# Optimization experiments

Measured on AMD Instinct MI355X. Metric: run time of the kernel, lower is better.

The kernel has to match this reference:

```python
import jax, jax.numpy as jnp
import numpy as np

# metaLinearLayer: per-sample weight W_b = left^T @ diag(meta_b) @ right.
# torch builds diag(meta)@eye@left then transposes and matmuls right, i.e.
# meta_weight[b] = (diag(meta_b) @ left).T @ right, shape (input_dim, out_dim).
# We apply it via associativity: (x @ left^T) * meta, then @ right -- same math,
# skipping the dense per-sample weight.

B, S, D_IN, D_OUT, P = 8, 4096, 2048, 2048, 256

def setup_inputs() -> dict:
    key = jax.random.key(0)
    ks = jax.random.split(key, 6)
    scale_l = (6.0 / D_IN) ** 0.5   # kaiming_uniform-ish magnitude
    scale_r = (6.0 / P) ** 0.5
    return {
        "input": jax.random.normal(ks[0], (B, S, D_IN), dtype=jnp.float32),
        "meta_input": jax.random.normal(ks[1], (B, P), dtype=jnp.float32),
        "left": jax.random.uniform(ks[2], (P, D_IN), dtype=jnp.float32, minval=-scale_l, maxval=scale_l),
        "right": jax.random.uniform(ks[3], (P, D_OUT), dtype=jnp.float32, minval=-scale_r, maxval=scale_r),
        "bias_w": jax.random.uniform(ks[4], (P, D_OUT), dtype=jnp.float32, minval=-scale_r, maxval=scale_r),
        "bias_b": jax.random.uniform(ks[5], (D_OUT,), dtype=jnp.float32, minval=-scale_r, maxval=scale_r),
    }

def reference(input, meta_input, left, right, bias_w, bias_b):
    # project input to rank-P space: [B,S,P]
    h = jnp.einsum('bsj,pj->bsp', input, left)
    # per-sample diagonal scaling by meta_input
    h = h * meta_input[:, None, :]
    # project to out_dim: [B,S,out_dim]
    out = jnp.einsum('bsp,pk->bsk', h, right)
    # meta bias = project2bias(meta_input), broadcast over seq
    meta_bias = meta_input @ bias_w + bias_b  # [B, out_dim]
    return out + meta_bias[:, None, :]
```

## Files before the change

### kernel.cpp

```cpp
#include <hip/hip_runtime.h>
#include <hip/hip_bf16.h>

#define B_    8
#define S_    4096
#define DIN   2048
#define DOUT  2048
#define P_    256
#define M_    (B_ * S_)

typedef __attribute__((ext_vector_type(4))) float f32x4;
typedef __attribute__((ext_vector_type(8))) short bf16x8;
typedef __attribute__((ext_vector_type(4))) short bf16x4;

static __device__ __forceinline__ short f2bs(float x) {
    __hip_bfloat16 h = __float2bfloat16(x);
    return *reinterpret_cast<short*>(&h);
}

__global__ __launch_bounds__(256)
void cvt_bf16_kernel(const float* __restrict__ src, short* __restrict__ dst, int n8) {
    int i = blockIdx.x * 256 + threadIdx.x;
    if (i >= n8) return;
    const float4* s = reinterpret_cast<const float4*>(src) + (size_t)i * 2;
    float4 a = s[0], b = s[1];
    bf16x8 o;
    o[0] = f2bs(a.x); o[1] = f2bs(a.y); o[2] = f2bs(a.z); o[3] = f2bs(a.w);
    o[4] = f2bs(b.x); o[5] = f2bs(b.y); o[6] = f2bs(b.z); o[7] = f2bs(b.w);
    *(reinterpret_cast<bf16x8*>(dst) + i) = o;
}

__global__ __launch_bounds__(256)
void transposeR_kernel(const float* __restrict__ R, short* __restrict__ Rt) {
    __shared__ float T[64][65];
    const int n0 = blockIdx.x * 64;
    const int k0 = blockIdx.y * 64;
    const int tid = threadIdx.x;
    #pragma unroll
    for (int e = 0; e < 16; ++e) {
        int idx = tid + e * 256;
        int r = idx >> 6, c = idx & 63;
        T[r][c] = R[(size_t)(k0 + r) * DOUT + n0 + c];
    }
    __syncthreads();
    #pragma unroll
    for (int e = 0; e < 4; ++e) {
        int g = tid + e * 256;
        int n = g >> 4, k4 = (g & 15) << 2;
        bf16x4 v;
        v[0] = f2bs(T[k4 + 0][n]); v[1] = f2bs(T[k4 + 1][n]);
        v[2] = f2bs(T[k4 + 2][n]); v[3] = f2bs(T[k4 + 3][n]);
        *reinterpret_cast<bf16x4*>(&Rt[(size_t)(n0 + n) * P_ + k0 + k4]) = v;
    }
}

__global__ __launch_bounds__(256)
void meta_bias_kernel(const float* __restrict__ meta,
                      const float* __restrict__ bias_w,
                      const float* __restrict__ bias_b,
                      float* __restrict__ mb) {
    int idx = blockIdx.x * 256 + threadIdx.x;
    int b = idx / DOUT;
    int k = idx - b * DOUT;
    const float* mrow = meta + b * P_;
    float acc = bias_b[k];
    #pragma unroll 8
    for (int p = 0; p < P_; ++p)
        acc = fmaf(mrow[p], bias_w[p * DOUT + k], acc);
    mb[idx] = acc;
}

template<int KTOT, int LDC, bool A_F32, bool META_EPI>
__global__ __launch_bounds__(512, 2)
void gemm_bt(const void* __restrict__ Ap,
             const short* __restrict__ Bp,
             const float* __restrict__ vvec,
             void* __restrict__ Cp) {
    constexpr int BM = 128, BN = 256, BK = 64;
    __shared__ short As[BM * BK];
    __shared__ short Bs[BN * BK];

    const int tid  = threadIdx.x;
    const int lane = tid & 63;
    const int w    = tid >> 6;
    const int wr   = w >> 2;
    const int wc   = w & 3;
    const int lm   = lane & 15;
    const int rg   = lane >> 4;
    const int r0   = blockIdx.x * BM;
    const int c0   = blockIdx.y * BN;
    const int bidx = r0 / S_;

    f32x4 acc[4][4] = {};

    const float* Af = (const float*)Ap;
    const short* Ab = (const short*)Ap;

    for (int k0 = 0; k0 < KTOT; k0 += BK) {
        #pragma unroll
        for (int e = 0; e < 2; ++e) {
            int c   = tid + e * 512;
            int row = c >> 3;
            int k8  = (c & 7) << 3;
            int off = ((row * BK + k8) * 2) ^ ((row & 7) << 4);
            bf16x8 o;
            if (A_F32) {
                const float* src = Af + (size_t)(r0 + row) * KTOT + k0 + k8;
                float4 v0 = *reinterpret_cast<const float4*>(src);
                float4 v1 = *reinterpret_cast<const float4*>(src + 4);
                o[0] = f2bs(v0.x); o[1] = f2bs(v0.y); o[2] = f2bs(v0.z); o[3] = f2bs(v0.w);
                o[4] = f2bs(v1.x); o[5] = f2bs(v1.y); o[6] = f2bs(v1.z); o[7] = f2bs(v1.w);
            } else {
                o = *reinterpret_cast<const bf16x8*>(Ab + (size_t)(r0 + row) * KTOT + k0 + k8);
            }
            *reinterpret_cast<bf16x8*>(reinterpret_cast<char*>(As) + off) = o;
        }
        #pragma unroll
        for (int e = 0; e < 4; ++e) {
            int c   = tid + e * 512;
            int row = c >> 3;
            int k8  = (c & 7) << 3;
            int off = ((row * BK + k8) * 2) ^ ((row & 7) << 4);
            bf16x8 o = *reinterpret_cast<const bf16x8*>(Bp + (size_t)(c0 + row) * KTOT + k0 + k8);
            *reinterpret_cast<bf16x8*>(reinterpret_cast<char*>(Bs) + off) = o;
        }
        __syncthreads();

        bf16x8 af[4][2], bfr[4][2];
        #pragma unroll
        for (int i = 0; i < 4; ++i)
            #pragma unroll
            for (int kk = 0; kk < 2; ++kk) {
                int m   = wr * 64 + i * 16 + lm;
                int off = ((m * BK + kk * 32 + rg * 8) * 2) ^ ((m & 7) << 4);
                af[i][kk] = *reinterpret_cast<const bf16x8*>(reinterpret_cast<const char*>(As) + off);
            }
        #pragma unroll
        for (int j = 0; j < 4; ++j)
            #pragma unroll
            for (int kk = 0; kk < 2; ++kk) {
                int n   = wc * 64 + j * 16 + lm;
                int off = ((n * BK + kk * 32 + rg * 8) * 2) ^ ((n & 7) << 4);
                bfr[j][kk] = *reinterpret_cast<const bf16x8*>(reinterpret_cast<const char*>(Bs) + off);
            }
        #pragma unroll
        for (int kk = 0; kk < 2; ++kk)
            #pragma unroll
            for (int i = 0; i < 4; ++i)
                #pragma unroll
                for (int j = 0; j < 4; ++j)
                    acc[i][j] = __builtin_amdgcn_mfma_f32_16x16x32_bf16(
                        af[i][kk], bfr[j][kk], acc[i][j], 0, 0, 0);
        __syncthreads();
    }

    if (META_EPI) {
        const float* mrow = vvec + bidx * P_;
        short* Hc = (short*)Cp;
        #pragma unroll
        for (int i = 0; i < 4; ++i) {
            int rbase = r0 + wr * 64 + i * 16 + rg * 4;
            #pragma unroll
            for (int j = 0; j < 4; ++j) {
                int col = c0 + wc * 64 + j * 16 + lm;
                float mv = mrow[col];
                #pragma unroll
                for (int q = 0; q < 4; ++q)
                    Hc[(size_t)(rbase + q) * LDC + col] = f2bs(acc[i][j][q] * mv);
            }
        }
    } else {
        const float* mbr = vvec + bidx * DOUT;
        float* Oc = (float*)Cp;
        #pragma unroll
        for (int i = 0; i < 4; ++i) {
            int rbase = r0 + wr * 64 + i * 16 + rg * 4;
            #pragma unroll
            for (int j = 0; j < 4; ++j) {
                int col = c0 + wc * 64 + j * 16 + lm;
                float bv = mbr[col];
                #pragma unroll
                for (int q = 0; q < 4; ++q)
                    Oc[(size_t)(rbase + q) * LDC + col] = acc[i][j][q] + bv;
            }
        }
    }
}

extern "C" void kernel_launch(void* const* d_in, const int* in_sizes, int n_in,
                              void* d_out, int out_size, void* d_ws, size_t ws_size,
                              hipStream_t stream) {
    const float* input  = (const float*)d_in[0];
    const float* meta   = (const float*)d_in[1];
    const float* left   = (const float*)d_in[2];
    const float* right  = (const float*)d_in[3];
    const float* bias_w = (const float*)d_in[4];
    const float* bias_b = (const float*)d_in[5];
    float* out = (float*)d_out;

    char* ws = (char*)d_ws;
    short* H  = (short*)ws;
    float* mb = (float*)(ws + 16777216);
    short* Lb = (short*)(ws + 16777216 + 65536);
    short* Rt = (short*)(ws + 16777216 + 65536 + 1048576);

    cvt_bf16_kernel<<<256, 256, 0, stream>>>(left, Lb, (P_ * DIN) / 8);
    transposeR_kernel<<<dim3(DOUT / 64, P_ / 64), 256, 0, stream>>>(right, Rt);
    meta_bias_kernel<<<(B_ * DOUT) / 256, 256, 0, stream>>>(meta, bias_w, bias_b, mb);

    gemm_bt<DIN, P_, true, true>
        <<<dim3(M_ / 128, 1), 512, 0, stream>>>(input, Lb, meta, H);

    gemm_bt<P_, DOUT, false, false>
        <<<dim3(M_ / 128, DOUT / 256), 512, 0, stream>>>(H, Rt, mb, out);
}
```

Before: 593.3 us.

## Pre-swizzle weight and H tiles and stream them with direct global-to-LDS loads

Weights and the intermediate H are written in a pre-tiled, pre-swizzled image layout, so the GEMM can copy 32KB/8KB tiles straight into LDS with global_load_lds instead of going through registers. The GEMM block shrinks to 64x256 with 256 threads at occupancy 3, and the meta-bias kernel is vectorised to float4. This removes register staging and address math for the B and H operands. In exchange the stage-1 GEMM now reads the whole left matrix for every 64 rows instead of every 128, and the stage-2 grid has twice as many blocks.

```diff
diff --git a/kernel.cpp b/kernel.cpp
--- a/kernel.cpp
+++ b/kernel.cpp
@@ -1,5 +1,6 @@
 #include <hip/hip_runtime.h>
 #include <hip/hip_bf16.h>
+#include <stdint.h>
 
 #define B_    8
 #define S_    4096
@@ -10,46 +11,62 @@
 
 typedef __attribute__((ext_vector_type(4))) float f32x4;
 typedef __attribute__((ext_vector_type(8))) short bf16x8;
-typedef __attribute__((ext_vector_type(4))) short bf16x4;
 
 static __device__ __forceinline__ short f2bs(float x) {
     __hip_bfloat16 h = __float2bfloat16(x);
     return *reinterpret_cast<short*>(&h);
 }
 
+static __device__ __forceinline__ void gld_lds16(const void* g, void* l) {
+    __builtin_amdgcn_global_load_lds(
+        (const __attribute__((address_space(1))) unsigned int*)(uintptr_t)g,
+        (__attribute__((address_space(3))) unsigned int*)(uintptr_t)l,
+        16, 0, 0);
+}
+
+#define SWZ(row, byteoff) ((byteoff) ^ (((row) & 7) << 4))
+
 __global__ __launch_bounds__(256)
-void cvt_bf16_kernel(const float* __restrict__ src, short* __restrict__ dst, int n8) {
-    int i = blockIdx.x * 256 + threadIdx.x;
-    if (i >= n8) return;
-    const float4* s = reinterpret_cast<const float4*>(src) + (size_t)i * 2;
-    float4 a = s[0], b = s[1];
+void prep_left(const float* __restrict__ L, char* __restrict__ Lsw) {
+    int g = blockIdx.x * 256 + threadIdx.x;
+    int row = g >> 8;
+    int c8  = g & 255;
+    int k = c8 * 8, kt = k >> 6, kk = k & 63;
+    const float* src = L + (size_t)row * DIN + k;
+    float4 v0 = *reinterpret_cast<const float4*>(src);
+    float4 v1 = *reinterpret_cast<const float4*>(src + 4);
     bf16x8 o;
-    o[0] = f2bs(a.x); o[1] = f2bs(a.y); o[2] = f2bs(a.z); o[3] = f2bs(a.w);
-    o[4] = f2bs(b.x); o[5] = f2bs(b.y); o[6] = f2bs(b.z); o[7] = f2bs(b.w);
-    *(reinterpret_cast<bf16x8*>(dst) + i) = o;
+    o[0]=f2bs(v0.x); o[1]=f2bs(v0.y); o[2]=f2bs(v0.z); o[3]=f2bs(v0.w);
+    o[4]=f2bs(v1.x); o[5]=f2bs(v1.y); o[6]=f2bs(v1.z); o[7]=f2bs(v1.w);
+    int off = kt * 32768 + SWZ(row, row * 128 + kk * 2);
+    *reinterpret_cast<bf16x8*>(Lsw + off) = o;
 }
 
 __global__ __launch_bounds__(256)
-void transposeR_kernel(const float* __restrict__ R, short* __restrict__ Rt) {
+void prep_right(const float* __restrict__ R, char* __restrict__ Rsw) {
     __shared__ float T[64][65];
     const int n0 = blockIdx.x * 64;
-    const int k0 = blockIdx.y * 64;
+    const int p0 = blockIdx.y * 64;
     const int tid = threadIdx.x;
     #pragma unroll
     for (int e = 0; e < 16; ++e) {
         int idx = tid + e * 256;
         int r = idx >> 6, c = idx & 63;
-        T[r][c] = R[(size_t)(k0 + r) * DOUT + n0 + c];
+        T[r][c] = R[(size_t)(p0 + r) * DOUT + n0 + c];
     }
     __syncthreads();
     #pragma unroll
-    for (int e = 0; e < 4; ++e) {
-        int g = tid + e * 256;
-        int n = g >> 4, k4 = (g & 15) << 2;
-        bf16x4 v;
-        v[0] = f2bs(T[k4 + 0][n]); v[1] = f2bs(T[k4 + 1][n]);
-        v[2] = f2bs(T[k4 + 2][n]); v[3] = f2bs(T[k4 + 3][n]);
-        *reinterpret_cast<bf16x4*>(&Rt[(size_t)(n0 + n) * P_ + k0 + k4]) = v;
+    for (int e = 0; e < 2; ++e) {
+        int cc = tid + e * 256;
+        int nl = cc >> 3, p8 = (cc & 7) * 8;
+        bf16x8 o;
+        #pragma unroll
+        for (int u = 0; u < 8; ++u) o[u] = f2bs(T[p8 + u][nl]);
+        int n = n0 + nl;
+        int nb = n >> 8, row = n & 255;
+        int kt = p0 >> 6, kk = p8;
+        int off = (nb * 4 + kt) * 32768 + SWZ(row, row * 128 + kk * 2);
+        *reinterpret_cast<bf16x8*>(Rsw + off) = o;
     }
 }
 
@@ -58,129 +75,138 @@
                       const float* __restrict__ bias_w,
                       const float* __restrict__ bias_b,
                       float* __restrict__ mb) {
-    int idx = blockIdx.x * 256 + threadIdx.x;
-    int b = idx / DOUT;
-    int k = idx - b * DOUT;
+    int g = blockIdx.x * 256 + threadIdx.x;
+    int b  = g >> 9;
+    int k4 = (g & 511) * 4;
     const float* mrow = meta + b * P_;
-    float acc = bias_b[k];
-    #pragma unroll 8
-    for (int p = 0; p < P_; ++p)
-        acc = fmaf(mrow[p], bias_w[p * DOUT + k], acc);
-    mb[idx] = acc;
-}
-
-template<int KTOT, int LDC, bool A_F32, bool META_EPI>
-__global__ __launch_bounds__(512, 2)
-void gemm_bt(const void* __restrict__ Ap,
-             const short* __restrict__ Bp,
-             const float* __restrict__ vvec,
-             void* __restrict__ Cp) {
-    constexpr int BM = 128, BN = 256, BK = 64;
-    __shared__ short As[BM * BK];
-    __shared__ short Bs[BN * BK];
+    float4 acc = *reinterpret_cast<const float4*>(&bias_b[k4]);
+    #pragma unroll 4
+    for (int p = 0; p < P_; ++p) {
+        float mval = mrow[p];
+        float4 wv = *reinterpret_cast<const float4*>(&bias_w[(size_t)p * DOUT + k4]);
+        acc.x = fmaf(mval, wv.x, acc.x);
+        acc.y = fmaf(mval, wv.y, acc.y);
+        acc.z = fmaf(mval, wv.z, acc.z);
+        acc.w = fmaf(mval, wv.w, acc.w);
+    }
+    *reinterpret_cast<float4*>(&mb[(size_t)b * DOUT + k4]) = acc;
+}
+
+template<bool S1>
+__global__ __launch_bounds__(256, 3)
+void gemm_mfma(const void* __restrict__ Ap,
+               const char* __restrict__ Bsw,
+               const float* __restrict__ vvec,
+               void* __restrict__ Cp) {
+    constexpr int KTOT = S1 ? DIN : P_;
+    constexpr int NK   = KTOT / 64;
+    __shared__ short As[64 * 64];
+    __shared__ short Bs[256 * 64];
 
     const int tid  = threadIdx.x;
     const int lane = tid & 63;
     const int w    = tid >> 6;
-    const int wr   = w >> 2;
-    const int wc   = w & 3;
     const int lm   = lane & 15;
     const int rg   = lane >> 4;
-    const int r0   = blockIdx.x * BM;
-    const int c0   = blockIdx.y * BN;
-    const int bidx = r0 / S_;
+    const int mblk = blockIdx.x;
+    const int r0   = mblk * 64;
+    const int c0   = S1 ? 0 : blockIdx.y * 256;
+    const int bidx = mblk >> 6;
 
     f32x4 acc[4][4] = {};
-
-    const float* Af = (const float*)Ap;
-    const short* Ab = (const short*)Ap;
-
-    for (int k0 = 0; k0 < KTOT; k0 += BK) {
-        #pragma unroll
-        for (int e = 0; e < 2; ++e) {
-            int c   = tid + e * 512;
-            int row = c >> 3;
-            int k8  = (c & 7) << 3;
-            int off = ((row * BK + k8) * 2) ^ ((row & 7) << 4);
-            bf16x8 o;
-            if (A_F32) {
-                const float* src = Af + (size_t)(r0 + row) * KTOT + k0 + k8;
+    const float* Xf  = (const float*)Ap;
+    const char* Himg = (const char*)Ap;
+    char* AsB = (char*)As;
+    char* BsB = (char*)Bs;
+
+    for (int kt = 0; kt < NK; ++kt) {
+        const char* bimg = Bsw + (size_t)(S1 ? kt : ((int)blockIdx.y * NK + kt)) * 32768;
+        #pragma unroll
+        for (int c = 0; c < 8; ++c)
+            gld_lds16(bimg + (w * 8 + c) * 1024 + lane * 16, BsB + (w * 8 + c) * 1024);
+        if (S1) {
+            #pragma unroll
+            for (int e = 0; e < 2; ++e) {
+                int row = (tid >> 3) + e * 32;
+                int k8  = (tid & 7) * 8;
+                const float* src = Xf + (size_t)(r0 + row) * DIN + kt * 64 + k8;
                 float4 v0 = *reinterpret_cast<const float4*>(src);
                 float4 v1 = *reinterpret_cast<const float4*>(src + 4);
-                o[0] = f2bs(v0.x); o[1] = f2bs(v0.y); o[2] = f2bs(v0.z); o[3] = f2bs(v0.w);
-                o[4] = f2bs(v1.x); o[5] = f2bs(v1.y); o[6] = f2bs(v1.z); o[7] = f2bs(v1.w);
-            } else {
-                o = *reinterpret_cast<const bf16x8*>(Ab + (size_t)(r0 + row) * KTOT + k0 + k8);
-            }
-            *reinterpret_cast<bf16x8*>(reinterpret_cast<char*>(As) + off) = o;
-        }
-        #pragma unroll
-        for (int e = 0; e < 4; ++e) {
-            int c   = tid + e * 512;
-            int row = c >> 3;
-            int k8  = (c & 7) << 3;
-            int off = ((row * BK + k8) * 2) ^ ((row & 7) << 4);
-            bf16x8 o = *reinterpret_cast<const bf16x8*>(Bp + (size_t)(c0 + row) * KTOT + k0 + k8);
-            *reinterpret_cast<bf16x8*>(reinterpret_cast<char*>(Bs) + off) = o;
+                bf16x8 o;
+                o[0]=f2bs(v0.x); o[1]=f2bs(v0.y); o[2]=f2bs(v0.z); o[3]=f2bs(v0.w);
+                o[4]=f2bs(v1.x); o[5]=f2bs(v1.y); o[6]=f2bs(v1.z); o[7]=f2bs(v1.w);
+                *reinterpret_cast<bf16x8*>(AsB + SWZ(row, row * 128 + k8 * 2)) = o;
+            }
+        } else {
+            const char* aimg = Himg + ((size_t)mblk * NK + kt) * 8192;
+            #pragma unroll
+            for (int c = 0; c < 2; ++c)
+                gld_lds16(aimg + (w * 2 + c) * 1024 + lane * 16, AsB + (w * 2 + c) * 1024);
         }
         __syncthreads();
 
-        bf16x8 af[4][2], bfr[4][2];
-        #pragma unroll
-        for (int i = 0; i < 4; ++i)
-            #pragma unroll
-            for (int kk = 0; kk < 2; ++kk) {
-                int m   = wr * 64 + i * 16 + lm;
-                int off = ((m * BK + kk * 32 + rg * 8) * 2) ^ ((m & 7) << 4);
-                af[i][kk] = *reinterpret_cast<const bf16x8*>(reinterpret_cast<const char*>(As) + off);
-            }
-        #pragma unroll
-        for (int j = 0; j < 4; ++j)
-            #pragma unroll
-            for (int kk = 0; kk < 2; ++kk) {
-                int n   = wc * 64 + j * 16 + lm;
-                int off = ((n * BK + kk * 32 + rg * 8) * 2) ^ ((n & 7) << 4);
-                bfr[j][kk] = *reinterpret_cast<const bf16x8*>(reinterpret_cast<const char*>(Bs) + off);
-            }
-        #pragma unroll
-        for (int kk = 0; kk < 2; ++kk)
+        #pragma unroll
+        for (int kk = 0; kk < 2; ++kk) {
+            bf16x8 af[4], bfr[4];
+            #pragma unroll
+            for (int i = 0; i < 4; ++i) {
+                int m = i * 16 + lm;
+                af[i] = *reinterpret_cast<const bf16x8*>(
+                    AsB + SWZ(m, m * 128 + (kk * 32 + rg * 8) * 2));
+            }
+            #pragma unroll
+            for (int j = 0; j < 4; ++j) {
+                int n = w * 64 + j * 16 + lm;
+                bfr[j] = *reinterpret_cast<const bf16x8*>(
+                    BsB + SWZ(n, n * 128 + (kk * 32 + rg * 8) * 2));
+            }
             #pragma unroll
             for (int i = 0; i < 4; ++i)
                 #pragma unroll
                 for (int j = 0; j < 4; ++j)
                     acc[i][j] = __builtin_amdgcn_mfma_f32_16x16x32_bf16(
-                        af[i][kk], bfr[j][kk], acc[i][j], 0, 0, 0);
+                        af[i], bfr[j], acc[i][j], 0, 0, 0);
+        }
         __syncthreads();
     }
 
-    if (META_EPI) {
+    if (S1) {
         const float* mrow = vvec + bidx * P_;
-        short* Hc = (short*)Cp;
+        char* Hout = (char*)Cp + (size_t)mblk * 32768;
+        float mv[4];
+        #pragma unroll
+        for (int j = 0; j < 4; ++j) mv[j] = mrow[w * 64 + j * 16 + lm];
         #pragma unroll
         for (int i = 0; i < 4; ++i) {
-            int rbase = r0 + wr * 64 + i * 16 + rg * 4;
+            int rb = i * 16 + rg * 4;
             #pragma unroll
             for (int j = 0; j < 4; ++j) {
-                int col = c0 + wc * 64 + j * 16 + lm;
-                float mv = mrow[col];
+                int p = w * 64 + j * 16 + lm;
+                int ktile = p >> 6, kk = p & 63;
                 #pragma unroll
-                for (int q = 0; q < 4; ++q)
-                    Hc[(size_t)(rbase + q) * LDC + col] = f2bs(acc[i][j][q] * mv);
+                for (int q = 0; q < 4; ++q) {
+                    int r = rb + q;
+                    int off = ktile * 8192 + SWZ(r, r * 128 + kk * 2);
+                    *reinterpret_cast<short*>(Hout + off) = f2bs(acc[i][j][q] * mv[j]);
+                }
             }
         }
     } else {
         const float* mbr = vvec + bidx * DOUT;
         float* Oc = (float*)Cp;
+        float bv[4];
+        #pragma unroll
+        for (int j = 0; j < 4; ++j) bv[j] = mbr[c0 + w * 64 + j * 16 + lm];
         #pragma unroll
         for (int i = 0; i < 4; ++i) {
-            int rbase = r0 + wr * 64 + i * 16 + rg * 4;
             #pragma unroll
             for (int j = 0; j < 4; ++j) {
-                int col = c0 + wc * 64 + j * 16 + lm;
-                float bv = mbr[col];
+                int col = c0 + w * 64 + j * 16 + lm;
                 #pragma unroll
-                for (int q = 0; q < 4; ++q)
-                    Oc[(size_t)(rbase + q) * LDC + col] = acc[i][j][q] + bv;
+                for (int q = 0; q < 4; ++q) {
+                    int row = r0 + i * 16 + rg * 4 + q;
+                    Oc[(size_t)row * DOUT + col] = acc[i][j][q] + bv[j];
+                }
             }
         }
     }
@@ -197,19 +223,17 @@
     const float* bias_b = (const float*)d_in[5];
     float* out = (float*)d_out;
 
-    char* ws = (char*)d_ws;
-    short* H  = (short*)ws;
+    char* ws  = (char*)d_ws;
+    char* Hsw = ws;
     float* mb = (float*)(ws + 16777216);
-    short* Lb = (short*)(ws + 16777216 + 65536);
-    short* Rt = (short*)(ws + 16777216 + 65536 + 1048576);
-
-    cvt_bf16_kernel<<<256, 256, 0, stream>>>(left, Lb, (P_ * DIN) / 8);
-    transposeR_kernel<<<dim3(DOUT / 64, P_ / 64), 256, 0, stream>>>(right, Rt);
-    meta_bias_kernel<<<(B_ * DOUT) / 256, 256, 0, stream>>>(meta, bias_w, bias_b, mb);
-
-    gemm_bt<DIN, P_, true, true>
-        <<<dim3(M_ / 128, 1), 512, 0, stream>>>(input, Lb, meta, H);
-
-    gemm_bt<P_, DOUT, false, false>
-        <<<dim3(M_ / 128, DOUT / 256), 512, 0, stream>>>(H, Rt, mb, out);
-}
+    char* Lsw = ws + 16777216 + 65536;
+    char* Rsw = Lsw + 1048576;
+
+    prep_left <<<256, 256, 0, stream>>>(left, Lsw);
+    prep_right<<<dim3(DOUT / 64, P_ / 64), 256, 0, stream>>>(right, Rsw);
+    meta_bias_kernel<<<16, 256, 0, stream>>>(meta, bias_w, bias_b, mb);
+
+    gemm_mfma<true><<<dim3(M_ / 64, 1), 256, 0, stream>>>(input, Lsw, meta, Hsw);
+
+    gemm_mfma<false><<<dim3(M_ / 64, DOUT / 256), 256, 0, stream>>>(Hsw, Rsw, mb, out);
+}
```

After: 569.0 us. 1.04x faster.
